# Optimization experiments

Hardware: AMD Instinct MI355X
Metric: run time of the kernel (lower is better)

## Reference

```python
import jax, jax.numpy as jnp
import numpy as np

B, N, C = 512, 252, 256  # N == C - 4 (class axis for torch-style CE over dim 1)


def setup_inputs() -> dict:
    key = jax.random.key(0)
    k1, k2, k3, k4, k5 = jax.random.split(key, 5)
    # output in (0,1): channel 0 feeds BCE (needs open interval), channel 3 gets sqrt'ed
    output = jax.random.uniform(k1, (B, N, C), dtype=jnp.float32) * 0.98 + 0.01
    # target: ch0 presence {0,1}, ch1..3 positive coords, ch4 integer class idx, rest filler
    presence = (jax.random.uniform(k2, (B, N)) < 0.7).astype(jnp.float32)
    coords = jax.random.uniform(k3, (B, N, 3), dtype=jnp.float32) * 0.9 + 0.05
    # per-batch permutation of class ids -> scatter is collision-free & deterministic
    cls = jax.vmap(lambda k: jax.random.permutation(k, N))(jax.random.split(k4, B))
    rest = jax.random.uniform(k5, (B, N, C - 5), dtype=jnp.float32)
    target = jnp.concatenate(
        [presence[:, :, None], coords, cls.astype(jnp.float32)[:, :, None], rest], axis=2
    )
    return {"output": output, "target": target}


def reference(output, target):
    Bb, Nn, Cc = output.shape
    # --- BCE on objectness (mean reduction) ---
    p = output[:, :, 0]
    t = target[:, :, 0]
    bce = -jnp.mean(t * jnp.log(p) + (1.0 - t) * jnp.log1p(-p))

    # --- vectorized masked scatter/reorder (replaces triple python loop) ---
    mask = t != 0  # [B, N]
    cls = target[:, :, 4].astype(jnp.int32)  # class index per box
    filtered = jnp.where(mask[:, :, None], output, 0.0)  # filtered_output
    bidx = jnp.arange(Bb)[:, None]
    idx = jnp.where(mask, cls, Nn)  # route absent boxes to dummy row Nn
    sorted_t = (
        jnp.zeros((Bb, Nn + 1, Cc), output.dtype).at[bidx, idx].set(target)[:, :Nn]
    )

    # --- CE: torch semantics, class axis = dim 1, spatial = dim 2 (size C-4 == N) ---
    tgt_cls = sorted_t[:, :, 4].astype(jnp.int32)  # [B, N] (spatial targets)
    logits = filtered[:, :, 4:]  # [B, N_classes, N_spatial]
    logp = jax.nn.log_softmax(logits, axis=1)
    picked = jnp.take_along_axis(logp, tgt_cls[:, None, :], axis=1)  # [B,1,N]
    ce = -jnp.mean(picked)

    # --- MSE terms ---
    Lx = jnp.mean((filtered[:, :, 1] - sorted_t[:, :, 1]) ** 2)
    Ly = jnp.mean((filtered[:, :, 2] - sorted_t[:, :, 2]) ** 2)
    Lwh = jnp.mean((jnp.sqrt(filtered[:, :, 3]) - jnp.sqrt(sorted_t[:, :, 3])) ** 2)
    mse = Lx + Ly + 2.0 * Lwh

    return 10.0 * mse + bce + 0.5 * (1.0 - bce) + ce
```

## Files before the change

kernel.cpp:

```cpp
#include <hip/hip_runtime.h>
#include <math.h>

#define BB 512
#define NN 252
#define CC 256

__global__ __launch_bounds__(256) void detloss_main(const float* __restrict__ outp,
                                                    const float* __restrict__ tgtp,
                                                    float* __restrict__ acc) {
    __shared__ float s_c1[NN], s_c2[NN], s_c3[NN];
    __shared__ float s_red[5];
    __shared__ unsigned char s_fill[NN];
    __shared__ unsigned char s_mask[NN];

    const int b = blockIdx.x;
    const int tid = threadIdx.x;
    const float* ob = outp + (size_t)b * NN * CC;
    const float* tb = tgtp + (size_t)b * NN * CC;

    if (tid < NN) { s_c1[tid] = 0.f; s_c2[tid] = 0.f; s_c3[tid] = 0.f; s_fill[tid] = 0; }
    if (tid < 5) s_red[tid] = 0.f;
    __syncthreads();

    float bce_c = 0.f, ce_c = 0.f, lx_c = 0.f, ly_c = 0.f, lwh_c = 0.f;
    float4 o4 = make_float4(0.f, 0.f, 0.f, 0.f);
    bool m = false;

    if (tid < NN) {
        const float4 t4 = *(const float4*)(tb + (size_t)tid * CC);
        const float tcls = tb[(size_t)tid * CC + 4];
        o4 = *(const float4*)(ob + (size_t)tid * CC);
        const float t0 = t4.x;
        const float p = o4.x;
        bce_c = -(t0 * __logf(p) + (1.f - t0) * log1pf(-p));
        m = (t0 != 0.f);
        s_mask[tid] = m ? 1 : 0;
        if (m) {
            const int j = (int)tcls;
            s_c1[j] = t4.y; s_c2[j] = t4.z; s_c3[j] = t4.w; s_fill[j] = 1;
        }
    }
    __syncthreads();

    if (tid < NN) {
        const float f1 = m ? o4.y : 0.f;
        const float f2 = m ? o4.z : 0.f;
        const float f3 = m ? o4.w : 0.f;
        const float d1 = f1 - s_c1[tid];
        const float d2 = f2 - s_c2[tid];
        const float d3 = sqrtf(f3) - sqrtf(s_c3[tid]);
        lx_c = d1 * d1; ly_c = d2 * d2; lwh_c = d3 * d3;

        const int k = tid;
        const float* cp = ob + 4 + k;
        float s = 0.f, diag = 0.f, x0 = 0.f;
        #pragma unroll 4
        for (int n = 0; n < NN; ++n) {
            const float v = cp[(size_t)n * CC];
            const float x = s_mask[n] ? v : 0.f;
            s += __expf(x);
            if (n == k) diag = x;
            if (n == 0) x0 = x;
        }
        const float lse = __logf(s);
        ce_c = lse - (s_fill[k] ? diag : x0);
    }

    #pragma unroll
    for (int off = 32; off > 0; off >>= 1) {
        bce_c += __shfl_down(bce_c, off);
        ce_c  += __shfl_down(ce_c,  off);
        lx_c  += __shfl_down(lx_c,  off);
        ly_c  += __shfl_down(ly_c,  off);
        lwh_c += __shfl_down(lwh_c, off);
    }
    if ((tid & 63) == 0) {
        atomicAdd(&s_red[0], bce_c);
        atomicAdd(&s_red[1], ce_c);
        atomicAdd(&s_red[2], lx_c);
        atomicAdd(&s_red[3], ly_c);
        atomicAdd(&s_red[4], lwh_c);
    }
    __syncthreads();
    if (tid < 5) atomicAdd(&acc[tid], s_red[tid]);
}

__global__ void detloss_final(const float* __restrict__ acc, float* __restrict__ outv) {
    const float inv = 1.0f / (float)(BB * NN);
    const float bce = acc[0] * inv;
    const float ce  = acc[1] * inv;
    const float lx  = acc[2] * inv;
    const float ly  = acc[3] * inv;
    const float lwh = acc[4] * inv;
    const float mse = lx + ly + 2.f * lwh;
    outv[0] = 10.f * mse + bce + 0.5f * (1.f - bce) + ce;
}

extern "C" void kernel_launch(void* const* d_in, const int* in_sizes, int n_in,
                              void* d_out, int out_size, void* d_ws, size_t ws_size,
                              hipStream_t stream) {
    const float* outp = (const float*)d_in[0];
    const float* tgtp = (const float*)d_in[1];
    float* acc = (float*)d_ws;
    hipMemsetAsync(acc, 0, 5 * sizeof(float), stream);
    detloss_main<<<BB, 256, 0, stream>>>(outp, tgtp, acc);
    detloss_final<<<1, 1, 0, stream>>>(acc, (float*)d_out);
}
```

Before: 265.1 us.

## Split column softmax across 16 waves with float4 loads and skip masked rows

Each block now runs 1024 threads. The per-column log-sum-exp over 252 rows is divided across 16 waves, and each lane reads a float4 of four columns per row, where before each thread walked one column with strided scalar loads. Rows whose objectness target is zero are skipped: each contributes exp(0)=1 to every column, which is added back through an absent-row count. Partial sums are combined through shared memory, with the diagonal and row-0 picks recorded during the pass. This adds a large shared buffer and an extra barrier, and the bigger block may lower occupancy.

```diff
diff --git a/kernel.cpp b/kernel.cpp
--- a/kernel.cpp
+++ b/kernel.cpp
@@ -4,22 +4,30 @@
 #define BB 512
 #define NN 252
 #define CC 256
+#define NW 16
 
-__global__ __launch_bounds__(256) void detloss_main(const float* __restrict__ outp,
-                                                    const float* __restrict__ tgtp,
-                                                    float* __restrict__ acc) {
+__global__ __launch_bounds__(1024) void detloss_main(const float* __restrict__ outp,
+                                                     const float* __restrict__ tgtp,
+                                                     float* __restrict__ acc) {
     __shared__ float s_c1[NN], s_c2[NN], s_c3[NN];
+    __shared__ float s_diag[NN], s_row0[NN];
+    __shared__ float s_part[NW * NN];
     __shared__ float s_red[5];
-    __shared__ unsigned char s_fill[NN];
-    __shared__ unsigned char s_mask[NN];
+    __shared__ int s_mask[NN];
+    __shared__ int s_fill[NN];
+    __shared__ int s_cnt;
 
     const int b = blockIdx.x;
     const int tid = threadIdx.x;
     const float* ob = outp + (size_t)b * NN * CC;
     const float* tb = tgtp + (size_t)b * NN * CC;
 
-    if (tid < NN) { s_c1[tid] = 0.f; s_c2[tid] = 0.f; s_c3[tid] = 0.f; s_fill[tid] = 0; }
+    if (tid < NN) {
+        s_c1[tid] = 0.f; s_c2[tid] = 0.f; s_c3[tid] = 0.f;
+        s_diag[tid] = 0.f; s_row0[tid] = 0.f; s_fill[tid] = 0;
+    }
     if (tid < 5) s_red[tid] = 0.f;
+    if (tid == 0) s_cnt = 0;
     __syncthreads();
 
     float bce_c = 0.f, ce_c = 0.f, lx_c = 0.f, ly_c = 0.f, lwh_c = 0.f;
@@ -31,13 +39,14 @@
         const float tcls = tb[(size_t)tid * CC + 4];
         o4 = *(const float4*)(ob + (size_t)tid * CC);
         const float t0 = t4.x;
-        const float p = o4.x;
-        bce_c = -(t0 * __logf(p) + (1.f - t0) * log1pf(-p));
+        bce_c = -(t0 * __logf(o4.x) + (1.f - t0) * log1pf(-o4.x));
         m = (t0 != 0.f);
         s_mask[tid] = m ? 1 : 0;
         if (m) {
             const int j = (int)tcls;
             s_c1[j] = t4.y; s_c2[j] = t4.z; s_c3[j] = t4.w; s_fill[j] = 1;
+        } else {
+            atomicAdd(&s_cnt, 1);
         }
     }
     __syncthreads();
@@ -50,20 +59,42 @@
         const float d2 = f2 - s_c2[tid];
         const float d3 = sqrtf(f3) - sqrtf(s_c3[tid]);
         lx_c = d1 * d1; ly_c = d2 * d2; lwh_c = d3 * d3;
+    }
 
-        const int k = tid;
-        const float* cp = ob + 4 + k;
-        float s = 0.f, diag = 0.f, x0 = 0.f;
+    const int wave = tid >> 6;
+    const int lane = tid & 63;
+    if (lane < 63) {
+        const float* base = ob + 4 + 4 * lane;
+        float4 sum = make_float4(0.f, 0.f, 0.f, 0.f);
         #pragma unroll 4
-        for (int n = 0; n < NN; ++n) {
-            const float v = cp[(size_t)n * CC];
-            const float x = s_mask[n] ? v : 0.f;
-            s += __expf(x);
-            if (n == k) diag = x;
-            if (n == 0) x0 = x;
+        for (int n = wave; n < NN; n += NW) {
+            if (s_mask[n]) {
+                const float4 v = *(const float4*)(base + (size_t)n * CC);
+                sum.x += __expf(v.x);
+                sum.y += __expf(v.y);
+                sum.z += __expf(v.z);
+                sum.w += __expf(v.w);
+                if ((n >> 2) == lane) {
+                    const int r = n & 3;
+                    s_diag[n] = (r == 0) ? v.x : (r == 1) ? v.y : (r == 2) ? v.z : v.w;
+                }
+                if (n == 0) {
+                    s_row0[4*lane+0] = v.x; s_row0[4*lane+1] = v.y;
+                    s_row0[4*lane+2] = v.z; s_row0[4*lane+3] = v.w;
+                }
+            }
         }
+        const int o = wave * NN + 4 * lane;
+        s_part[o+0] = sum.x; s_part[o+1] = sum.y; s_part[o+2] = sum.z; s_part[o+3] = sum.w;
+    }
+    __syncthreads();
+
+    if (tid < NN) {
+        float s = (float)s_cnt;
+        #pragma unroll
+        for (int w = 0; w < NW; ++w) s += s_part[w * NN + tid];
         const float lse = __logf(s);
-        ce_c = lse - (s_fill[k] ? diag : x0);
+        ce_c = lse - (s_fill[tid] ? s_diag[tid] : s_row0[tid]);
     }
 
     #pragma unroll
@@ -74,7 +105,7 @@
         ly_c  += __shfl_down(ly_c,  off);
         lwh_c += __shfl_down(lwh_c, off);
     }
-    if ((tid & 63) == 0) {
+    if (lane == 0) {
         atomicAdd(&s_red[0], bce_c);
         atomicAdd(&s_red[1], ce_c);
         atomicAdd(&s_red[2], lx_c);
@@ -103,6 +134,6 @@
     const float* tgtp = (const float*)d_in[1];
     float* acc = (float*)d_ws;
     hipMemsetAsync(acc, 0, 5 * sizeof(float), stream);
-    detloss_main<<<BB, 256, 0, stream>>>(outp, tgtp, acc);
+    detloss_main<<<BB, 1024, 0, stream>>>(outp, tgtp, acc);
     detloss_final<<<1, 1, 0, stream>>>(acc, (float*)d_out);
 }
```

Result: faster. 249.1 us (-6.0%).
